# Performance work log

Hardware: AMD Instinct MI355X
Metric: run time of the kernel (lower is better)

Reference implementation:

```python
import jax, jax.numpy as jnp
import numpy as np

B, S, D_MODEL, H = 2, 2048, 512, 8
DH = D_MODEL // H  # dim per head
NEG_INF = 1e9


def setup_inputs() -> dict:
    key = jax.random.key(0)
    ks = jax.random.split(key, 8)
    sc = 0.05
    return {
        "query": jax.random.normal(ks[0], (B, S, D_MODEL), jnp.float32),
        "key": jax.random.normal(ks[1], (B, S, D_MODEL), jnp.float32),
        "value": jax.random.normal(ks[2], (B, S, D_MODEL), jnp.float32),
        "mask": jnp.zeros((B, 1, S, S), jnp.float32),
        "wq": jax.random.normal(ks[3], (D_MODEL, D_MODEL), jnp.float32) * sc,
        "bq": jnp.zeros((D_MODEL,), jnp.float32),
        "wk": jax.random.normal(ks[4], (D_MODEL, D_MODEL), jnp.float32) * sc,
        "bk": jnp.zeros((D_MODEL,), jnp.float32),
        "wv": jax.random.normal(ks[5], (D_MODEL, D_MODEL), jnp.float32) * sc,
        "bv": jnp.zeros((D_MODEL,), jnp.float32),
        "wo": jax.random.normal(ks[6], (D_MODEL, D_MODEL), jnp.float32) * sc,
        "bo": jnp.zeros((D_MODEL,), jnp.float32),
    }


def _split_heads(x):
    # (B, S, D_MODEL) -> (B, H, S, DH)
    b, s, _ = x.shape
    return x.reshape(b, s, H, DH).transpose(0, 2, 1, 3)


def reference(query, key, value, mask, wq, bq, wk, bk, wv, bv, wo, bo):
    q = _split_heads(query @ wq + bq)
    k = _split_heads(key @ wk + bk)
    v = _split_heads(value @ wv + bv)
    # scaled dot-product attention; full (B, H, S, S) scores as in original
    scores = jnp.einsum("bhqd,bhkd->bhqk", q, k) / jnp.sqrt(jnp.float32(DH))
    scores = scores + mask * (-NEG_INF)
    weights = jax.nn.softmax(scores, axis=-1)  # dropout inactive (rate=0 / eval)
    attn = jnp.einsum("bhqk,bhkd->bhqd", weights, v)
    # merge heads: (B, H, S, DH) -> (B, S, D_MODEL)
    b = attn.shape[0]
    merged = attn.transpose(0, 2, 1, 3).reshape(b, -1, D_MODEL)
    return merged @ wo + bo
```

## Files before the change

kernel.cpp:

```cpp
#include <hip/hip_runtime.h>
#include <hip/hip_bf16.h>

typedef unsigned short u16;
typedef unsigned int u32;
typedef __bf16 bf16x8 __attribute__((ext_vector_type(8)));
typedef float f32x4 __attribute__((ext_vector_type(4)));
typedef u16 u16x8 __attribute__((ext_vector_type(8)));
typedef u32 u32x2 __attribute__((ext_vector_type(2)));

#define S_LEN 2048
#define DMODEL 512
#define NHEAD 8
#define DHEAD 64
#define QSCALE 0.1803368801111204f
#define MASKC 1.4426950409e9f
#define RESCALE_THR 8.0f

static __device__ __forceinline__ u16 f2bf(float f) {
    union { float f; unsigned u; } cv; cv.f = f;
    unsigned u = cv.u;
    return (u16)((u + 0x7fffu + ((u >> 16) & 1u)) >> 16);
}
static __device__ __forceinline__ u32 pk2bf(float a, float b) {
    union { __hip_bfloat162 h; u32 u; } cv;
    float2 f2; f2.x = a; f2.y = b;
    cv.h = __float22bfloat162_rn(f2);
    return cv.u;
}
static __device__ __forceinline__ bf16x8 ld8(const u16* p) {
    return *(const bf16x8*)p;
}
static __device__ __forceinline__ float fmax3(float a, float b, float c) {
    return __builtin_fmaxf(__builtin_fmaxf(a, b), c);
}
static __device__ __forceinline__ void gll16(const void* g, void* l) {
    __builtin_amdgcn_global_load_lds(
        (const __attribute__((address_space(1))) void*)g,
        (__attribute__((address_space(3))) void*)l, 16, 0, 0);
}

__global__ __launch_bounds__(256) void prep_kernel(
    const float* __restrict__ q, const float* __restrict__ k, const float* __restrict__ v,
    const float* __restrict__ w0, const float* __restrict__ w1,
    const float* __restrict__ w2, const float* __restrict__ w3,
    const float* __restrict__ mask,
    u16* __restrict__ Aqkv, u16* __restrict__ wtall, int* __restrict__ flags) {
    const int p = blockIdx.x;
    const int tid = threadIdx.x;
    __shared__ float t[32][33];
    __shared__ int wred[4];
    if (p < 3072) {
        const int z = p >> 10, px = p & 1023;
        const float* in = (z == 0) ? q : (z == 1) ? k : v;
        u16* o = Aqkv + (long)z * 2097152;
        long i = ((long)px * 256 + tid) * 8;
        f32x4 a = *(const f32x4*)(in + i);
        f32x4 b = *(const f32x4*)(in + i + 4);
        u16x8 r;
#pragma unroll
        for (int j = 0; j < 4; ++j) { r[j] = f2bf(a[j]); r[4 + j] = f2bf(b[j]); }
        *(u16x8*)(o + i) = r;
    } else if (p < 4096) {
        const int p2 = p - 3072;
        const int z = p2 >> 8, rem = p2 & 255, by = rem >> 4, bx = rem & 15;
        const float* in = (z == 0) ? w0 : (z == 1) ? w1 : (z == 2) ? w2 : w3;
        u16* o = wtall + (long)(((z + 1) & 3)) * 262144;
        const int tx = tid & 31, ty = tid >> 5;
#pragma unroll
        for (int i = 0; i < 4; ++i)
            t[ty + 8 * i][tx] = in[(by * 32 + ty + 8 * i) * DMODEL + bx * 32 + tx];
        __syncthreads();
#pragma unroll
        for (int i = 0; i < 4; ++i)
            o[(bx * 32 + ty + 8 * i) * DMODEL + by * 32 + tx] = f2bf(t[tx][ty + 8 * i]);
    } else {
        const int bid = p - 4096;
        const int b = bid >> 10, qt = (bid >> 5) & 31, kt = bid & 31;
        const int r = tid >> 2, cs = tid & 3;
        const float* mp = mask + ((long)(b * S_LEN + qt * 64 + r)) * S_LEN + kt * 64 + cs * 16;
        int nz = 0;
#pragma unroll
        for (int j = 0; j < 4; ++j) {
            f32x4 a = *(const f32x4*)(mp + j * 4);
            nz |= (a[0] != 0.f) | (a[1] != 0.f) | (a[2] != 0.f) | (a[3] != 0.f);
        }
        unsigned long long ball = __ballot(nz);
        if ((tid & 63) == 0) wred[tid >> 6] = (ball != 0ull) ? 1 : 0;
        __syncthreads();
        if (tid == 0) flags[bid] = wred[0] | wred[1] | wred[2] | wred[3];
    }
}

template <bool F32OUT, int TM>
static __device__ __forceinline__ void store_c(f32x4 (&acc)[TM][2],
                                               const float* __restrict__ bias,
                                               void* __restrict__ Cp, float oscale,
                                               bool vtout, int m0, int n0, int cidx, int kg) {
    if (vtout) {
        const int bb = m0 >> 11;
#pragma unroll
        for (int j = 0; j < 2; ++j) {
            int col = n0 + j * 16 + cidx;
            float bv = bias[col];
            u16* vt = (u16*)Cp + (((long)(bb * 8 + (col >> 6))) * 64 + (col & 63)) * S_LEN;
#pragma unroll
            for (int i = 0; i < TM; ++i) {
                int s = (m0 + i * 16 + kg * 4) & (S_LEN - 1);
                u32x2 d;
                d[0] = pk2bf(acc[i][j][0] + bv, acc[i][j][1] + bv);
                d[1] = pk2bf(acc[i][j][2] + bv, acc[i][j][3] + bv);
                *(u32x2*)(vt + s) = d;
            }
        }
        return;
    }
#pragma unroll
    for (int j = 0; j < 2; ++j) {
        int col = n0 + j * 16 + cidx;
        float bv = bias[col];
#pragma unroll
        for (int i = 0; i < TM; ++i) {
#pragma unroll
            for (int r = 0; r < 4; ++r) {
                int row = m0 + i * 16 + kg * 4 + r;
                float val = (acc[i][j][r] + bv) * oscale;
                if (F32OUT) {
                    ((float*)Cp)[(long)row * DMODEL + col] = val;
                } else {
                    ((u16*)Cp)[(long)row * DMODEL + col] = f2bf(val);
                }
            }
        }
    }
}

template <int BM, bool F32OUT>
static __device__ __forceinline__ void gemm_lds(const u16* __restrict__ Ag,
                                                const u16* __restrict__ Wg,
                                                const float* __restrict__ bias,
                                                void* __restrict__ Cp, float oscale,
                                                bool vtout, int bx, int by) {
    constexpr int MR = BM / 32;
    constexpr int ACH = BM * 4;
    constexpr int TOT = ACH + 256;
    constexpr int NCH = (TOT + 255) / 256;
    __shared__ __align__(16) u16 As[2][BM][32];
    __shared__ __align__(16) u16 Bs[2][64][32];

    const int tid = threadIdx.x;
    const int lane = tid & 63;
    const int wave = tid >> 6;
    const int wr = wave >> 1, wc = wave & 1;
    const int cidx = lane & 15;
    const int kg = lane >> 4;

    const u16* gsrc[NCH];
    u16* ldst[NCH][2];
    bool val[NCH];
#pragma unroll
    for (int j = 0; j < NCH; ++j) {
        int c = tid + 256 * j;
        val[j] = (c < TOT);
        int cc = val[j] ? c : 0;
        if (cc < ACH) {
            int r = cc >> 2, s = cc & 3;
            int sg = s ^ ((r >> 1) & 3);
            gsrc[j] = Ag + (long)(by * BM + r) * DMODEL + sg * 8;
            ldst[j][0] = &As[0][0][0] + cc * 8;
            ldst[j][1] = &As[1][0][0] + cc * 8;
        } else {
            int c2 = cc - ACH;
            int r = c2 >> 2, s = c2 & 3;
            int sg = s ^ ((r >> 1) & 3);
            gsrc[j] = Wg + (long)(bx * 64 + r) * DMODEL + sg * 8;
            ldst[j][0] = &Bs[0][0][0] + c2 * 8;
            ldst[j][1] = &Bs[1][0][0] + c2 * 8;
        }
    }

#pragma unroll
    for (int j = 0; j < NCH; ++j) if (val[j]) gll16(gsrc[j], ldst[j][0]);
    __syncthreads();

    const f32x4 fz = {0.f, 0.f, 0.f, 0.f};
    f32x4 acc[MR][2];
#pragma unroll
    for (int i = 0; i < MR; ++i)
#pragma unroll
        for (int j = 0; j < 2; ++j) acc[i][j] = fz;

    const int mw = (BM >= 64) ? wr * (BM / 2) : wr * 16;
    const int nw = wc * 32;

#pragma unroll 2
    for (int t = 0; t < 16; ++t) {
        const int cur = t & 1;
        if (t + 1 < 16) {
#pragma unroll
            for (int j = 0; j < NCH; ++j)
                if (val[j]) gll16(gsrc[j] + (t + 1) * 32, ldst[j][cur ^ 1]);
        }
        bf16x8 a[MR], b[2];
#pragma unroll
        for (int i = 0; i < MR; ++i) {
            int rl = mw + i * 16 + cidx;
            a[i] = ld8(&As[cur][rl][(kg ^ ((rl >> 1) & 3)) * 8]);
        }
#pragma unroll
        for (int j = 0; j < 2; ++j) {
            int rl = nw + j * 16 + cidx;
            b[j] = ld8(&Bs[cur][rl][(kg ^ ((rl >> 1) & 3)) * 8]);
        }
        __builtin_amdgcn_s_setprio(1);
#pragma unroll
        for (int i = 0; i < MR; ++i)
#pragma unroll
            for (int j = 0; j < 2; ++j)
                acc[i][j] = __builtin_amdgcn_mfma_f32_16x16x32_bf16(a[i], b[j], acc[i][j], 0, 0, 0);
        __builtin_amdgcn_s_setprio(0);
        __syncthreads();
    }

    store_c<F32OUT, MR>(acc, bias, Cp, oscale, vtout, by * BM + mw, bx * 64 + nw, cidx, kg);
}

static __device__ __forceinline__ void xcd_swizzle(int gridX, int gridY, int& bx, int& by) {
    const int flat = blockIdx.x + gridX * blockIdx.y;
    const int xcd = flat & 7;
    const int j = flat >> 3;
    by = xcd * (gridY >> 3) + j / gridX;
    bx = j % gridX;
}

__global__ __launch_bounds__(256) void qkv_gemm_kernel(
    const u16* __restrict__ Aqkv,
    const u16* __restrict__ wtall,
    const float* __restrict__ bq, const float* __restrict__ bk, const float* __restrict__ bv,
    u16* __restrict__ Q, u16* __restrict__ K, u16* __restrict__ Vt) {
    const u16* A = Aqkv + (long)blockIdx.z * 2097152;
    const u16* W = wtall + (long)(blockIdx.z + 1) * 262144;
    const float* b;
    u16* C;
    float sc = 1.f;
    bool vt = false;
    if (blockIdx.z == 0) { b = bq; C = Q; sc = QSCALE; }
    else if (blockIdx.z == 1) { b = bk; C = K; }
    else { b = bv; C = Vt; vt = true; }
    int bx, by;
    xcd_swizzle(8, 32, bx, by);
    gemm_lds<128, false>(A, W, b, C, sc, vt, bx, by);
}

__global__ __launch_bounds__(256) void out_gemm_kernel(const u16* __restrict__ A,
                                                       const u16* __restrict__ Wt,
                                                       const float* __restrict__ bias,
                                                       float* __restrict__ C) {
    int bx, by;
    xcd_swizzle(8, 128, bx, by);
    gemm_lds<32, true>(A, Wt, bias, C, 1.f, false, bx, by);
}

__global__ __launch_bounds__(256) void attn_kernel(const u16* __restrict__ Q,
                                                   const u16* __restrict__ K,
                                                   const u16* __restrict__ Vt,
                                                   const float* __restrict__ mask,
                                                   const int* __restrict__ flags,
                                                   u16* __restrict__ Ab) {
    const int tid = threadIdx.x;
    const int lane = tid & 63;
    const int wave = tid >> 6;
    const int cidx = lane & 15;
    const int kg = lane >> 4;
    const int flat = blockIdx.x + 32 * blockIdx.y;
    const int F = (flat & 7) * 64 + (flat >> 3);
    const int qt = F & 31;
    const int bh = F >> 5;
    const int b = bh >> 3, h = bh & 7;
    const int q0 = qt * 64 + wave * 16;

    __shared__ __align__(16) u16 kt_lds[2][64 * 64];
    __shared__ __align__(16) u16 vt_lds[2][64 * 64];
    __shared__ u16 p_lds[4][16 * 64];
    u16* pw = p_lds[wave];

    const long qbase = ((long)(b * S_LEN + q0 + cidx)) * DMODEL + h * DHEAD + kg * 8;
    bf16x8 aq0 = ld8(Q + qbase);
    bf16x8 aq1 = ld8(Q + qbase + 32);

    bf16x8 onesf;
    {
        u16x8 t8;
        u16 ob = (cidx == 0) ? (u16)0x3F80 : (u16)0;
#pragma unroll
        for (int j = 0; j < 8; ++j) t8[j] = ob;
        onesf = *(bf16x8*)&t8;
    }

    const f32x4 fz = {0.f, 0.f, 0.f, 0.f};
    f32x4 acc[4];
#pragma unroll
    for (int nt = 0; nt < 4; ++nt) acc[nt] = fz;
    f32x4 accL = fz;
    float mrow = -1e30f;

    const int krow0 = tid >> 3, kseg0 = tid & 7;
    const int krow1 = krow0 + 32;
    const u16* kgbase = K + ((long)(b * S_LEN)) * DMODEL + h * DHEAD;
    const u16* vgbase = Vt + ((long)bh * DHEAD) * S_LEN;
    const int sg0 = kseg0 ^ (krow0 & 7);
    const int sg1 = kseg0 ^ (krow1 & 7);
    const int* flagrow = flags + b * 1024 + qt * 32;
    const int NIT = S_LEN / 64;

    const u16* kp0 = kgbase + (long)krow0 * DMODEL + sg0 * 8;
    const u16* kp1 = kgbase + (long)krow1 * DMODEL + sg1 * 8;
    const u16* vp0 = vgbase + (long)krow0 * S_LEN + sg0 * 8;
    const u16* vp1 = vgbase + (long)krow1 * S_LEN + sg1 * 8;

    gll16(kp0, &kt_lds[0][tid * 8]);
    gll16(kp1, &kt_lds[0][2048 + tid * 8]);
    gll16(vp0, &vt_lds[0][tid * 8]);
    gll16(vp1, &vt_lds[0][2048 + tid * 8]);
    __syncthreads();

#define ATTN_TILE(IT, CUR)                                                                 \
    {                                                                                      \
        if ((IT) + 1 < NIT) {                                                              \
            const int tn = ((IT) + 1) * 64;                                                \
            u16* kn = kt_lds[(CUR) ^ 1];                                                   \
            u16* vn = vt_lds[(CUR) ^ 1];                                                   \
            gll16(kp0 + (long)tn * DMODEL, &kn[tid * 8]);                                  \
            gll16(kp1 + (long)tn * DMODEL, &kn[2048 + tid * 8]);                           \
            gll16(vp0 + tn, &vn[tid * 8]);                                                 \
            gll16(vp1 + tn, &vn[2048 + tid * 8]);                                          \
        }                                                                                  \
        const int flg = flagrow[(IT)];                                                     \
        const u16* kb = kt_lds[(CUR)];                                                     \
        const u16* vb = vt_lds[(CUR)];                                                     \
        f32x4 sacc[4];                                                                     \
        _Pragma("unroll")                                                                  \
        for (int ct = 0; ct < 4; ++ct) sacc[ct] = fz;                                      \
        __builtin_amdgcn_s_setprio(1);                                                     \
        _Pragma("unroll")                                                                  \
        for (int ct = 0; ct < 4; ++ct) {                                                   \
            int r = ct * 16 + cidx;                                                        \
            bf16x8 kv0 = ld8(&kb[r * 64 + ((kg ^ (r & 7)) << 3)]);                         \
            bf16x8 kv1 = ld8(&kb[r * 64 + (((4 ^ kg) ^ (r & 7)) << 3)]);                   \
            sacc[ct] = __builtin_amdgcn_mfma_f32_16x16x32_bf16(kv0, aq0, sacc[ct], 0, 0, 0); \
            sacc[ct] = __builtin_amdgcn_mfma_f32_16x16x32_bf16(kv1, aq1, sacc[ct], 0, 0, 0); \
        }                                                                                  \
        __builtin_amdgcn_s_setprio(0);                                                     \
        if (flg) {                                                                         \
            const float* mb = mask + ((long)(b * S_LEN + q0 + cidx)) * S_LEN + (IT) * 64 + kg * 4; \
            _Pragma("unroll")                                                              \
            for (int ct = 0; ct < 4; ++ct) {                                               \
                f32x4 mv = *(const f32x4*)(mb + ct * 16);                                  \
                _Pragma("unroll")                                                          \
                for (int r = 0; r < 4; ++r) sacc[ct][r] -= MASKC * mv[r];                  \
            }                                                                              \
        }                                                                                  \
        float t0 = fmax3(sacc[0][0], sacc[0][1], sacc[0][2]);                              \
        float t1 = fmax3(sacc[0][3], sacc[1][0], sacc[1][1]);                              \
        float t2 = fmax3(sacc[1][2], sacc[1][3], sacc[2][0]);                              \
        float t3 = fmax3(sacc[2][1], sacc[2][2], sacc[2][3]);                              \
        float t4 = fmax3(sacc[3][0], sacc[3][1], sacc[3][2]);                              \
        float mxl = __builtin_fmaxf(fmax3(fmax3(t0, t1, t2), t3, t4), sacc[3][3]);         \
        if (__any(mxl > mrow + RESCALE_THR)) {                                             \
            float mx = fmaxf(mxl, __shfl_xor(mxl, 16));                                    \
            mx = fmaxf(mx, __shfl_xor(mx, 32));                                            \
            float mnew = fmaxf(mrow, mx);                                                  \
            float alpha = __builtin_amdgcn_exp2f(mrow - mnew);                             \
            mrow = mnew;                                                                   \
            accL = accL * alpha;                                                           \
            _Pragma("unroll")                                                              \
            for (int nt = 0; nt < 4; ++nt) acc[nt] = acc[nt] * alpha;                      \
        }                                                                                  \
        _Pragma("unroll")                                                                  \
        for (int ct = 0; ct < 4; ++ct)                                                     \
            _Pragma("unroll")                                                              \
            for (int r = 0; r < 4; ++r)                                                    \
                sacc[ct][r] = __builtin_amdgcn_exp2f(sacc[ct][r] - mrow);                  \
        _Pragma("unroll")                                                                  \
        for (int ct = 0; ct < 4; ++ct) {                                                   \
            u32x2 d;                                                                       \
            d[0] = pk2bf(sacc[ct][0], sacc[ct][1]);                                        \
            d[1] = pk2bf(sacc[ct][2], sacc[ct][3]);                                        \
            int blk = 2 * ct + (kg >> 1);                                                  \
            *(u32x2*)&pw[cidx * 64 + ((blk ^ (cidx & 7)) << 3) + (kg & 1) * 4] = d;        \
        }                                                                                  \
        bf16x8 pf0 = ld8(&pw[cidx * 64 + ((kg ^ (cidx & 7)) << 3)]);                       \
        bf16x8 pf1 = ld8(&pw[cidx * 64 + (((4 ^ kg) ^ (cidx & 7)) << 3)]);                 \
        __builtin_amdgcn_s_setprio(1);                                                     \
        _Pragma("unroll")                                                                  \
        for (int nt = 0; nt < 4; ++nt) {                                                   \
            int rr = nt * 16 + cidx;                                                       \
            bf16x8 v0 = ld8(&vb[rr * 64 + ((kg ^ (rr & 7)) << 3)]);                        \
            bf16x8 v1 = ld8(&vb[rr * 64 + (((4 ^ kg) ^ (rr & 7)) << 3)]);                  \
            acc[nt] = __builtin_amdgcn_mfma_f32_16x16x32_bf16(v0, pf0, acc[nt], 0, 0, 0);  \
            acc[nt] = __builtin_amdgcn_mfma_f32_16x16x32_bf16(v1, pf1, acc[nt], 0, 0, 0);  \
        }                                                                                  \
        accL = __builtin_amdgcn_mfma_f32_16x16x32_bf16(onesf, pf0, accL, 0, 0, 0);         \
        accL = __builtin_amdgcn_mfma_f32_16x16x32_bf16(onesf, pf1, accL, 0, 0, 0);         \
        __builtin_amdgcn_s_setprio(0);                                                     \
        __syncthreads();                \
    }

    for (int it = 0; it < NIT; it += 2) {
        ATTN_TILE(it, 0)
        ATTN_TILE(it + 1, 1)
    }
#undef ATTN_TILE

    float Lb = __shfl(accL[0], cidx);
    float invL = 1.f / Lb;
    const long abase = ((long)(b * S_LEN + q0 + cidx)) * DMODEL + h * DHEAD;
#pragma unroll
    for (int nt = 0; nt < 4; ++nt) {
        u32x2 d;
        d[0] = pk2bf(acc[nt][0] * invL, acc[nt][1] * invL);
        d[1] = pk2bf(acc[nt][2] * invL, acc[nt][3] * invL);
        *(u32x2*)(Ab + abase + nt * 16 + kg * 4) = d;
    }
}

extern "C" void kernel_launch(void* const* d_in, const int* in_sizes, int n_in,
                              void* d_out, int out_size, void* d_ws, size_t ws_size,
                              hipStream_t stream) {
    const float* q_in = (const float*)d_in[0];
    const float* k_in = (const float*)d_in[1];
    const float* v_in = (const float*)d_in[2];
    const float* mask = (const float*)d_in[3];
    const float* wq = (const float*)d_in[4];
    const float* bq = (const float*)d_in[5];
    const float* wk = (const float*)d_in[6];
    const float* bk = (const float*)d_in[7];
    const float* wv = (const float*)d_in[8];
    const float* bv = (const float*)d_in[9];
    const float* wo = (const float*)d_in[10];
    const float* bo = (const float*)d_in[11];

    u16* ws = (u16*)d_ws;
    u16* Qb = ws;
    u16* Kb = Qb + 2097152;
    u16* Vt = Kb + 2097152;
    u16* wtall = Vt + 2097152;
    u16* Sreg = wtall + 4 * 262144;
    u16* Ab = Sreg + 3 * 2097152;
    int* mflags = (int*)(Ab + 2097152);

    prep_kernel<<<6144, 256, 0, stream>>>(q_in, k_in, v_in, wq, wk, wv, wo, mask,
                                          Sreg, wtall, mflags);
    qkv_gemm_kernel<<<dim3(8, 32, 3), 256, 0, stream>>>(Sreg, wtall, bq, bk, bv, Qb, Kb, Vt);
    attn_kernel<<<dim3(32, 16), 256, 0, stream>>>(Qb, Kb, Vt, mask, mflags, Ab);
    out_gemm_kernel<<<dim3(8, 128), 256, 0, stream>>>(Ab, wtall, bo, (float*)d_out);
}
```

Measured before the change: 171.9 us.

## Use single-wave attention blocks loading K/V fragments directly into registers

The attention kernel now runs one wave per block on 16 query rows, loading K and V MFMA fragments straight from global memory into registers instead of staging 64x64 tiles in LDS. K is double-buffered in registers and the per-tile __syncthreads is removed. This cuts LDS traffic and block-level synchronisation, but four waves that used to share each staged K/V tile now each fetch it separately through L2/L1. It also raises register pressure.

```diff
diff --git a/kernel.cpp b/kernel.cpp
--- a/kernel.cpp
+++ b/kernel.cpp
@@ -260,28 +260,23 @@
     gemm_lds<32, true>(A, Wt, bias, C, 1.f, false, bx, by);
 }
 
-__global__ __launch_bounds__(256) void attn_kernel(const u16* __restrict__ Q,
-                                                   const u16* __restrict__ K,
-                                                   const u16* __restrict__ Vt,
-                                                   const float* __restrict__ mask,
-                                                   const int* __restrict__ flags,
-                                                   u16* __restrict__ Ab) {
-    const int tid = threadIdx.x;
-    const int lane = tid & 63;
-    const int wave = tid >> 6;
+__global__ __launch_bounds__(64) void attn_kernel(const u16* __restrict__ Q,
+                                                  const u16* __restrict__ K,
+                                                  const u16* __restrict__ Vt,
+                                                  const float* __restrict__ mask,
+                                                  const int* __restrict__ flags,
+                                                  u16* __restrict__ Ab) {
+    const int lane = threadIdx.x;
     const int cidx = lane & 15;
     const int kg = lane >> 4;
-    const int flat = blockIdx.x + 32 * blockIdx.y;
-    const int F = (flat & 7) * 64 + (flat >> 3);
-    const int qt = F & 31;
-    const int bh = F >> 5;
+    const int flat = blockIdx.x + 128 * blockIdx.y;
+    const int F = (flat & 7) * 256 + (flat >> 3);
+    const int qt = F & 127;
+    const int bh = F >> 7;
     const int b = bh >> 3, h = bh & 7;
-    const int q0 = qt * 64 + wave * 16;
-
-    __shared__ __align__(16) u16 kt_lds[2][64 * 64];
-    __shared__ __align__(16) u16 vt_lds[2][64 * 64];
-    __shared__ u16 p_lds[4][16 * 64];
-    u16* pw = p_lds[wave];
+    const int q0 = qt * 16;
+
+    __shared__ u16 pw[16 * 64];
 
     const long qbase = ((long)(b * S_LEN + q0 + cidx)) * DMODEL + h * DHEAD + kg * 8;
     bf16x8 aq0 = ld8(Q + qbase);
@@ -303,53 +298,58 @@
     f32x4 accL = fz;
     float mrow = -1e30f;
 
-    const int krow0 = tid >> 3, kseg0 = tid & 7;
-    const int krow1 = krow0 + 32;
-    const u16* kgbase = K + ((long)(b * S_LEN)) * DMODEL + h * DHEAD;
-    const u16* vgbase = Vt + ((long)bh * DHEAD) * S_LEN;
-    const int sg0 = kseg0 ^ (krow0 & 7);
-    const int sg1 = kseg0 ^ (krow1 & 7);
-    const int* flagrow = flags + b * 1024 + qt * 32;
+    const u16* kbp = K + ((long)(b * S_LEN)) * DMODEL + h * DHEAD;
+    const u16* vbp = Vt + ((long)bh * DHEAD) * S_LEN;
+    const u16* kp[4];
+    const u16* vp[4];
+#pragma unroll
+    for (int t = 0; t < 4; ++t) {
+        kp[t] = kbp + (long)(t * 16 + cidx) * DMODEL + kg * 8;
+        vp[t] = vbp + (long)(t * 16 + cidx) * S_LEN + kg * 8;
+    }
+    const int* flagrow = flags + b * 1024 + (qt >> 2) * 32;
     const int NIT = S_LEN / 64;
 
-    const u16* kp0 = kgbase + (long)krow0 * DMODEL + sg0 * 8;
-    const u16* kp1 = kgbase + (long)krow1 * DMODEL + sg1 * 8;
-    const u16* vp0 = vgbase + (long)krow0 * S_LEN + sg0 * 8;
-    const u16* vp1 = vgbase + (long)krow1 * S_LEN + sg1 * 8;
-
-    gll16(kp0, &kt_lds[0][tid * 8]);
-    gll16(kp1, &kt_lds[0][2048 + tid * 8]);
-    gll16(vp0, &vt_lds[0][tid * 8]);
-    gll16(vp1, &vt_lds[0][2048 + tid * 8]);
-    __syncthreads();
+    bf16x8 kf[2][8];
+#pragma unroll
+    for (int ct = 0; ct < 4; ++ct) {
+        kf[0][2 * ct] = ld8(kp[ct]);
+        kf[0][2 * ct + 1] = ld8(kp[ct] + 32);
+    }
 
 #define ATTN_TILE(IT, CUR)                                                                 \
     {                                                                                      \
         if ((IT) + 1 < NIT) {                                                              \
-            const int tn = ((IT) + 1) * 64;                                                \
-            u16* kn = kt_lds[(CUR) ^ 1];                                                   \
-            u16* vn = vt_lds[(CUR) ^ 1];                                                   \
-            gll16(kp0 + (long)tn * DMODEL, &kn[tid * 8]);                                  \
-            gll16(kp1 + (long)tn * DMODEL, &kn[2048 + tid * 8]);                           \
-            gll16(vp0 + tn, &vn[tid * 8]);                                                 \
-            gll16(vp1 + tn, &vn[2048 + tid * 8]);                                          \
-        }                                                                                  \
-        const int flg = flagrow[(IT)];                                                     \
-        const u16* kb = kt_lds[(CUR)];                                                     \
-        const u16* vb = vt_lds[(CUR)];                                                     \
+            const long tn = (long)(((IT) + 1) * 64) * DMODEL;                              \
+            _Pragma("unroll")                                                              \
+            for (int ct = 0; ct < 4; ++ct) {                                               \
+                kf[(CUR) ^ 1][2 * ct] = ld8(kp[ct] + tn);                                  \
+                kf[(CUR) ^ 1][2 * ct + 1] = ld8(kp[ct] + tn + 32);                         \
+            }                                                                              \
+        }                                                                                  \
         f32x4 sacc[4];                                                                     \
         _Pragma("unroll")                                                                  \
         for (int ct = 0; ct < 4; ++ct) sacc[ct] = fz;                                      \
         __builtin_amdgcn_s_setprio(1);                                                     \
         _Pragma("unroll")                                                                  \
         for (int ct = 0; ct < 4; ++ct) {                                                   \
-            int r = ct * 16 + cidx;                                                        \
-            bf16x8 kv0 = ld8(&kb[r * 64 + ((kg ^ (r & 7)) << 3)]);                         \
-            bf16x8 kv1 = ld8(&kb[r * 64 + (((4 ^ kg) ^ (r & 7)) << 3)]);                   \
-            sacc[ct] = __builtin_amdgcn_mfma_f32_16x16x32_bf16(kv0, aq0, sacc[ct], 0, 0, 0); \
-            sacc[ct] = __builtin_amdgcn_mfma_f32_16x16x32_bf16(kv1, aq1, sacc[ct], 0, 0, 0); \
+            sacc[ct] = __builtin_amdgcn_mfma_f32_16x16x32_bf16(kf[(CUR)][2 * ct], aq0,     \
+                                                               sacc[ct], 0, 0, 0);         \
+            sacc[ct] = __builtin_amdgcn_mfma_f32_16x16x32_bf16(kf[(CUR)][2 * ct + 1], aq1, \
+                                                               sacc[ct], 0, 0, 0);         \
         }                                                                                  \
         __builtin_amdgcn_s_setprio(0);                                                     \
+                            \
+        bf16x8 vf[8];                                                                      \
+        {                                                                                  \
+            const int vo = (IT) * 64;                                                      \
+            _Pragma("unroll")                                                              \
+            for (int nt = 0; nt < 4; ++nt) {                                               \
+                vf[2 * nt] = ld8(vp[nt] + vo);                                             \
+                vf[2 * nt + 1] = ld8(vp[nt] + vo + 32);                                    \
+            }                                                                              \
+        }                                                                                  \
+        const int flg = flagrow[(IT)];                                                     \
         if (flg) {                                                                         \
             const float* mb = mask + ((long)(b * S_LEN + q0 + cidx)) * S_LEN + (IT) * 64 + kg * 4; \
             _Pragma("unroll")                                                              \
@@ -393,16 +393,12 @@
         __builtin_amdgcn_s_setprio(1);                                                     \
         _Pragma("unroll")                                                                  \
         for (int nt = 0; nt < 4; ++nt) {                                                   \
-            int rr = nt * 16 + cidx;                                                       \
-            bf16x8 v0 = ld8(&vb[rr * 64 + ((kg ^ (rr & 7)) << 3)]);                        \
-            bf16x8 v1 = ld8(&vb[rr * 64 + (((4 ^ kg) ^ (rr & 7)) << 3)]);                  \
-            acc[nt] = __builtin_amdgcn_mfma_f32_16x16x32_bf16(v0, pf0, acc[nt], 0, 0, 0);  \
-            acc[nt] = __builtin_amdgcn_mfma_f32_16x16x32_bf16(v1, pf1, acc[nt], 0, 0, 0);  \
+            acc[nt] = __builtin_amdgcn_mfma_f32_16x16x32_bf16(vf[2 * nt], pf0, acc[nt], 0, 0, 0); \
+            acc[nt] = __builtin_amdgcn_mfma_f32_16x16x32_bf16(vf[2 * nt + 1], pf1, acc[nt], 0, 0, 0); \
         }                                                                                  \
         accL = __builtin_amdgcn_mfma_f32_16x16x32_bf16(onesf, pf0, accL, 0, 0, 0);         \
         accL = __builtin_amdgcn_mfma_f32_16x16x32_bf16(onesf, pf1, accL, 0, 0, 0);         \
         __builtin_amdgcn_s_setprio(0);                                                     \
-        __syncthreads();                \
     }
 
     for (int it = 0; it < NIT; it += 2) {
@@ -451,6 +447,6 @@
     prep_kernel<<<6144, 256, 0, stream>>>(q_in, k_in, v_in, wq, wk, wv, wo, mask,
                                           Sreg, wtall, mflags);
     qkv_gemm_kernel<<<dim3(8, 32, 3), 256, 0, stream>>>(Sreg, wtall, bq, bk, bv, Qb, Kb, Vt);
-    attn_kernel<<<dim3(32, 16), 256, 0, stream>>>(Qb, Kb, Vt, mask, mflags, Ab);
+    attn_kernel<<<dim3(128, 16), 64, 0, stream>>>(Qb, Kb, Vt, mask, mflags, Ab);
     out_gemm_kernel<<<dim3(8, 128), 256, 0, stream>>>(Ab, wtall, bo, (float*)d_out);
 }
```

Result: slower. 247.9 us (+44.2%).
